# Kernel optimization log

Hardware: AMD Instinct MI355X
Metric: run time of the kernel (lower is better)

## Reference

```python
import jax, jax.numpy as jnp
import numpy as np

B, S, T = 1024, 1024, 32  # batch, seq_len, num_tags


def setup_inputs() -> dict:
    key = jax.random.key(0)
    k1, k2, k3, k4 = jax.random.split(key, 4)
    logits = jax.random.normal(k1, (B, S, T), dtype=jnp.float32)
    transitions = jax.random.normal(k2, (T, T), dtype=jnp.float32)
    tags = jax.random.randint(k3, (B, S), 0, T)
    lengths = jax.random.randint(k4, (B,), 1, S + 1)
    return {"logits": logits, "transitions": transitions, "tags": tags, "lengths": lengths}


def _forward_alg(logits, transitions):
    # viterbi_0 = logits[:, 0, :]; then for t>=1:
    # v_next[b, j] = logsumexp_i(v[b, i] + trans[i, j]) + logits[b, t, j]
    v0 = logits[:, 0, :]  # (B, T)
    emits = jnp.swapaxes(logits[:, 1:, :], 0, 1)  # (S-1, B, T)

    def step(v, emit_t):
        v_next = jax.nn.logsumexp(v[:, :, None] + transitions[None, :, :], axis=1) + emit_t
        return v_next, None

    v_final, _ = jax.lax.scan(step, v0, emits)
    return jax.nn.logsumexp(v_final, axis=1)  # (B,)


def _score_sentence(logits, transitions, tags, lengths):
    # emission scores of gold tags, masked to t < length (note: original ignores
    # lengths in the forward algorithm but uses them here, faithfully reproduced)
    emit = jnp.take_along_axis(logits, tags[:, :, None], axis=2)[..., 0]  # (B, S)
    pos = jnp.arange(S)
    emit_mask = (pos[None, :] < lengths[:, None]).astype(logits.dtype)
    score = jnp.sum(emit * emit_mask, axis=1)
    # transition scores trans[tags[t-1], tags[t]] for 1 <= t < length
    trans_sc = transitions[tags[:, :-1], tags[:, 1:]]  # (B, S-1)
    trans_mask = (pos[None, 1:] < lengths[:, None]).astype(logits.dtype)
    score = score + jnp.sum(trans_sc * trans_mask, axis=1)
    return score  # (B,)


def reference(logits, transitions, tags, lengths):
    log_z = _forward_alg(logits, transitions)
    gold = _score_sentence(logits, transitions, tags, lengths)
    return jnp.mean(log_z - gold)
```

## Files before the change

kernel.cpp:

```cpp
#include <hip/hip_runtime.h>

#define NB 1024
#define NS 1024
#define NT 32
#define L2E 1.44269504088896340736f
#define LN2 0.69314718055994530942f

typedef short        bfrag  __attribute__((ext_vector_type(8)));
typedef float        cfrag  __attribute__((ext_vector_type(16)));
typedef __bf16       bf16x2 __attribute__((ext_vector_type(2)));
typedef float        f32x8  __attribute__((ext_vector_type(8)));
typedef float        f32x4  __attribute__((ext_vector_type(4)));
typedef float        f32x2  __attribute__((ext_vector_type(2)));
typedef unsigned int u32;
typedef unsigned int u32x2v __attribute__((ext_vector_type(2)));
typedef unsigned int u32x4  __attribute__((ext_vector_type(4)));

__device__ __forceinline__ float fexp2(float x){ return __builtin_amdgcn_exp2f(x); }
__device__ __forceinline__ float flog2(float x){ return __builtin_amdgcn_logf(x); }

__device__ __forceinline__ u32 pkbf_rne(float a, float b){
    f32x2 t; t.x = a; t.y = b;
    return __builtin_bit_cast(u32, __builtin_convertvector(t, bf16x2));
}
__device__ __forceinline__ u32 pkbf_t(float a, float b){
    return __builtin_amdgcn_perm(__builtin_bit_cast(u32, b),
                                 __builtin_bit_cast(u32, a), 0x07060302u);
}
__device__ __forceinline__ bfrag mk_afrag(f32x8 v){
    u32x4 r;
    r[0] = pkbf_rne(v[0], v[1]); r[1] = pkbf_rne(v[2], v[3]);
    r[2] = pkbf_rne(v[4], v[5]); r[3] = pkbf_rne(v[6], v[7]);
    return __builtin_bit_cast(bfrag, r);
}

#if __has_builtin(__builtin_amdgcn_permlane32_swap)
#define HAVE_PLSWAP 1
#else
#define HAVE_PLSWAP 0
#endif

__device__ __forceinline__ void half_swap(u32 &x, u32 &y, int h){
#if HAVE_PLSWAP
    u32x2v r = __builtin_amdgcn_permlane32_swap(x, y, false, false);
    x = r[0]; y = r[1];
#else
    u32 X  = __shfl_xor(h ? x : y, 32, 64);
    u32 nx = h ? X : x;
    u32 ny = h ? y : X;
    x = nx; y = ny;
#endif
}

template<int N> struct ic { static constexpr int value = N; };
union accu { cfrag c; f32x2 p[8]; };
union q4u  { f32x4 v; f32x2 p[2]; };

__global__ __launch_bounds__(256, 8) void crf_chunk(
    const float* __restrict__ logits, const float* __restrict__ trans,
    u32* __restrict__ wmat, float* __restrict__ woff)
{
    __shared__ __align__(16) float dscall[4 * 512];

    const int tid = threadIdx.x;
    const int wv  = tid >> 6, lt = tid & 63;
    const int m   = lt & 31,  h  = lt >> 5;
    const int bc  = blockIdx.x * 4 + wv;
    const int b   = bc >> 3,  c  = bc & 7;
    float* dsc = dscall + wv * 512;

    const float* base = logits + (size_t)b * NS * NT;

    f32x8 Et0, Et1;
    #pragma unroll
    for (int j = 0; j < 8; j++){
        Et0[j] = fexp2(L2E * trans[(     8*h + j)*NT + m]);
        Et1[j] = fexp2(L2E * trans[(16 + 8*h + j)*NT + m]);
    }
    const bfrag A0f = mk_afrag(Et0);
    const bfrag A1f = mk_afrag(Et1);

    u32x4 B0v, B1v;
    #pragma unroll
    for (int d = 0; d < 4; d++){
        int k0 = 8*h + 2*d;      u32 v = 0;
        if (k0     == m) v |= 0x3F80u;
        if (k0 + 1 == m) v |= 0x3F800000u;
        B0v[d] = v;
        int k1 = 16 + 8*h + 2*d; v = 0;
        if (k1     == m) v |= 0x3F80u;
        if (k1 + 1 == m) v |= 0x3F800000u;
        B1v[d] = v;
    }

    cfrag zacc;
    #pragma unroll
    for (int q = 0; q < 16; q++) zacc[q] = 0.0f;

    int   offi = 0;
    float exf  = 0.0f;
    const int tbeg = c*128 + 1;

    float eA[4], eB[4];

    auto issue = [&](float (&e)[4], int k){
        const int t0 = tbeg + k*8 + 4*h;
        #pragma unroll
        for (int i = 0; i < 4; i++){
            int t = t0 + i; t = t > (NS-1) ? (NS-1) : t;
            e[i] = base[t*NT + m];
        }
    };
    auto commit = [&](float (&e)[4], int k){
        float* sp = dsc + (k & 1)*256 + (4*h)*32 + m;
        float a0 = (h == 0) ? -exf : 0.0f;
        sp[0]    = fexp2(fmaf(L2E, e[0], a0));
        sp[32]   = fexp2(L2E * e[1]);
        sp[64]   = fexp2(L2E * e[2]);
        sp[96]   = fexp2(L2E * e[3]);
    };

    auto exref = [&](float ref)->int{
        u32 xb = __builtin_bit_cast(u32, ref);
        u32 xf = __builtin_amdgcn_readfirstlane(xb);
        int ex = (int)((xf >> 23) & 0xFFu) - 127;
        return ex < -120 ? -120 : (ex > 120 ? 120 : ex);
    };

    auto procN = [&](int k, bool defer, auto nstc){
        constexpr int NST = decltype(nstc)::value;
        const float* db = dsc + (k & 1)*256 + 4*h;
        #pragma unroll
        for (int i = 0; i < NST; i++){
            accu acc;
            acc.c = __builtin_amdgcn_mfma_f32_32x32x16_bf16(
                        A0f, __builtin_bit_cast(bfrag, B0v), zacc, 0, 0, 0);
            acc.c = __builtin_amdgcn_mfma_f32_32x32x16_bf16(
                        A1f, __builtin_bit_cast(bfrag, B1v), acc.c, 0, 0, 0);

            q4u d0, d1, d2, d3;
            d0.v = *(const f32x4*)(db + i*32 +  0);
            d1.v = *(const f32x4*)(db + i*32 +  8);
            d2.v = *(const f32x4*)(db + i*32 + 16);
            d3.v = *(const f32x4*)(db + i*32 + 24);
            acc.p[0] *= d0.p[0]; acc.p[1] *= d0.p[1];
            acc.p[2] *= d1.p[0]; acc.p[3] *= d1.p[1];
            acc.p[4] *= d2.p[0]; acc.p[5] *= d2.p[1];
            acc.p[6] *= d3.p[0]; acc.p[7] *= d3.p[1];

            if (i == 3){
                int ex = exref(fmaxf(acc.c[0], acc.c[8]));
                offi += ex;
                f32x2 s2;
                s2.x = s2.y = __builtin_bit_cast(float, (u32)(127 - ex) << 23);
                #pragma unroll
                for (int q = 0; q < 8; q++) acc.p[q] *= s2;
            }
            if (i == 7 && defer){
                int ex = exref(fmaxf(acc.c[0], acc.c[8]));
                offi += ex;
                exf = (float)ex;
            }

            u32 P0 = pkbf_t(acc.c[0],  acc.c[1]),  P1 = pkbf_t(acc.c[2],  acc.c[3]);
            u32 P2 = pkbf_t(acc.c[4],  acc.c[5]),  P3 = pkbf_t(acc.c[6],  acc.c[7]);
            u32 P4 = pkbf_t(acc.c[8],  acc.c[9]),  P5 = pkbf_t(acc.c[10], acc.c[11]);
            u32 P6 = pkbf_t(acc.c[12], acc.c[13]), P7 = pkbf_t(acc.c[14], acc.c[15]);
            half_swap(P0, P2, h); half_swap(P1, P3, h);
            half_swap(P4, P6, h); half_swap(P5, P7, h);
            B0v[0]=P0; B0v[1]=P1; B0v[2]=P2; B0v[3]=P3;
            B1v[0]=P4; B1v[1]=P5; B1v[2]=P6; B1v[3]=P7;
        }
    };

    issue(eA, 0); commit(eA, 0);
    #pragma unroll 1
    for (int k = 0; k < 14; k += 2){
        issue(eB, k + 1);
        procN(k, true, ic<8>{});
        commit(eB, k + 1);
        issue(eA, k + 2);
        procN(k + 1, true, ic<8>{});
        commit(eA, k + 2);
    }
    issue(eB, 15);
    procN(14, true, ic<8>{});
    commit(eB, 15);
    if (c != 7) procN(15, false, ic<8>{});
    else        procN(15, false, ic<7>{});

    const size_t mb = (size_t)bc * 512;
    #pragma unroll
    for (int d = 0; d < 4; d++){
        wmat[mb + d*64 + lt]     = B0v[d];
        wmat[mb + (4+d)*64 + lt] = B1v[d];
    }
    if (lt == 0) woff[bc] = (float)offi;
}

__global__ __launch_bounds__(256) void crf_gold(
    const float* __restrict__ logits, const float* __restrict__ trans,
    const int* __restrict__ tags, const int* __restrict__ lens,
    float* __restrict__ out)
{
    __shared__ __align__(16) float ldsT[NT*NT];
    __shared__ __align__(16) int   ldsTag[NS];
    __shared__ float red[4];

    const int tid = threadIdx.x;
    const int b   = blockIdx.x;
    const int len = lens[b];
    const float* lgb = logits + (size_t)b * NS * NT;

    ((float4*)ldsT)[tid]  = ((const float4*)trans)[tid];
    ((int4*)ldsTag)[tid]  = ((const int4*)(tags + (size_t)b * NS))[tid];
    __syncthreads();

    const int t0 = tid * 4;
    int4 tgv = ((const int4*)ldsTag)[tid];
    int  prv = ldsTag[tid == 0 ? 0 : t0 - 1];
    int tgs[5] = {prv, tgv.x, tgv.y, tgv.z, tgv.w};

    float g = 0.0f;
    #pragma unroll
    for (int i = 0; i < 4; i++){
        int t = t0 + i;
        if (t < len){
            float e  = lgb[t*NT + tgs[i+1]];
            float tr = (t >= 1) ? ldsT[tgs[i]*NT + tgs[i+1]] : 0.0f;
            g += e + tr;
        }
    }

    #pragma unroll
    for (int d = 1; d < 64; d <<= 1) g += __shfl_xor(g, d, 64);
    if ((tid & 63) == 0) red[tid >> 6] = g;
    __syncthreads();
    if (tid == 0){
        float gs = red[0] + red[1] + red[2] + red[3];
        atomicAdd(out, -gs * (1.0f / (float)NB));
    }
}

__global__ __launch_bounds__(64) void crf_combine(
    const float* __restrict__ logits,
    const u32* __restrict__ wmat, const float* __restrict__ woff,
    float* __restrict__ out)
{
    __shared__ __align__(16) float ldsU[NT];

    const int tid = threadIdx.x;
    const int m   = tid & 31;
    const int b   = blockIdx.x;
    const float* lgb = logits + (size_t)b * NS * NT;

    float offs[8];
    #pragma unroll
    for (int cc = 0; cc < 8; cc++) offs[cc] = woff[b*8 + cc];

    float v    = fexp2(L2E * lgb[m]);
    float voff = 0.0f;

    const int n  = m;
    const int f  = n >> 4;
    const int hh = (n >> 3) & 1;
    const int di = f*4 + ((n >> 1) & 3);

    auto ldrow = [&](int cc, uint4 (&md)[8]){
        const uint4* mp = (const uint4*)(wmat + (size_t)(b*8 + cc)*512 + di*64 + hh*32);
        #pragma unroll
        for (int qq = 0; qq < 8; qq++) md[qq] = mp[qq];
    };

    uint4 mdA[8], mdB[8];
    ldrow(0, mdA);

    #pragma unroll
    for (int cc = 0; cc < 8; cc++){
        uint4 (&cur)[8] = (cc & 1) ? mdB : mdA;
        uint4 (&nxt)[8] = (cc & 1) ? mdA : mdB;
        if (cc < 7) ldrow(cc + 1, nxt);

        float w  = flog2(v) + offs[cc];
        float mw = w;
        #pragma unroll
        for (int d = 1; d <= 16; d <<= 1) mw = fmaxf(mw, __shfl_xor(mw, d, 64));
        float u = fexp2(w - mw);
        if (tid < 32) ldsU[m] = u;
        __syncthreads();

        float acc = 0.0f;
        #pragma unroll
        for (int qq = 0; qq < 8; qq++){
            uint4  md = cur[qq];
            float4 uu = ((const float4*)ldsU)[qq];
            float e0 = __builtin_bit_cast(float, (n&1) ? (md.x & 0xFFFF0000u) : (md.x << 16));
            float e1 = __builtin_bit_cast(float, (n&1) ? (md.y & 0xFFFF0000u) : (md.y << 16));
            float e2 = __builtin_bit_cast(float, (n&1) ? (md.z & 0xFFFF0000u) : (md.z << 16));
            float e3 = __builtin_bit_cast(float, (n&1) ? (md.w & 0xFFFF0000u) : (md.w << 16));
            acc = fmaf(e0, uu.x, acc);
            acc = fmaf(e1, uu.y, acc);
            acc = fmaf(e2, uu.z, acc);
            acc = fmaf(e3, uu.w, acc);
        }
        v = acc;
        voff += mw;
        __syncthreads();
    }

    float s = v;
    #pragma unroll
    for (int d = 1; d <= 16; d <<= 1) s += __shfl_xor(s, d, 64);
    if (tid == 0){
        float logz = LN2 * (voff + flog2(s));
        atomicAdd(out, logz * (1.0f / (float)NB));
    }
}

extern "C" void kernel_launch(void* const* d_in, const int* in_sizes, int n_in,
                              void* d_out, int out_size, void* d_ws, size_t ws_size,
                              hipStream_t stream) {
    const float* logits = (const float*)d_in[0];
    const float* trans  = (const float*)d_in[1];
    const int*   tags   = (const int*)d_in[2];
    const int*   lens   = (const int*)d_in[3];

    u32*   wmat = (u32*)d_ws;
    float* woff = (float*)(wmat + 8192*512);

    hipMemsetAsync(d_out, 0, sizeof(float), stream);
    crf_chunk  <<<2048, 256, 0, stream>>>(logits, trans, wmat, woff);
    crf_gold   <<<1024, 256, 0, stream>>>(logits, trans, tags, lens, (float*)d_out);
    crf_combine<<<1024,  64, 0, stream>>>(logits, wmat, woff, (float*)d_out);
}
```

Measured before the change: 278.6 us.

## Fuse gold-score into chunk kernel and drop half-swap via permuted tag order

Removes the separate gold-score kernel. Its emission and transition sums are now accumulated inside the chunk kernel from the logits already loaded there, and the per-chunk partials go to a workspace buffer that the combine kernel reads. The tag index is also permuted (rho) in the transition A-fragment, the identity B init and the combine readout. This lets the MFMA output be packed straight back into B operands, dropping the cross-half permlane swaps on the serial recurrence path. The cost is extra scattered tag and transition loads inside the latency-critical chunk loop, plus a reliance on the permutation being exactly right.

Result: slower. 309.0 us (+10.9%).

```diff
diff --git a/kernel.cpp b/kernel.cpp
--- a/kernel.cpp
+++ b/kernel.cpp
@@ -13,7 +13,6 @@
 typedef float        f32x4  __attribute__((ext_vector_type(4)));
 typedef float        f32x2  __attribute__((ext_vector_type(2)));
 typedef unsigned int u32;
-typedef unsigned int u32x2v __attribute__((ext_vector_type(2)));
 typedef unsigned int u32x4  __attribute__((ext_vector_type(4)));
 
 __device__ __forceinline__ float fexp2(float x){ return __builtin_amdgcn_exp2f(x); }
@@ -34,22 +33,9 @@
     return __builtin_bit_cast(bfrag, r);
 }
 
-#if __has_builtin(__builtin_amdgcn_permlane32_swap)
-#define HAVE_PLSWAP 1
-#else
-#define HAVE_PLSWAP 0
-#endif
-
-__device__ __forceinline__ void half_swap(u32 &x, u32 &y, int h){
-#if HAVE_PLSWAP
-    u32x2v r = __builtin_amdgcn_permlane32_swap(x, y, false, false);
-    x = r[0]; y = r[1];
-#else
-    u32 X  = __shfl_xor(h ? x : y, 32, 64);
-    u32 nx = h ? X : x;
-    u32 ny = h ? y : X;
-    x = nx; y = ny;
-#endif
+__device__ __forceinline__ int rho(int k){
+    int bb = (k >> 2) & 3;
+    return (bb == 1 || bb == 2) ? (k ^ 12) : k;
 }
 
 template<int N> struct ic { static constexpr int value = N; };
@@ -58,7 +44,8 @@
 
 __global__ __launch_bounds__(256, 8) void crf_chunk(
     const float* __restrict__ logits, const float* __restrict__ trans,
-    u32* __restrict__ wmat, float* __restrict__ woff)
+    const int* __restrict__ tags, const int* __restrict__ lens,
+    u32* __restrict__ wmat, float* __restrict__ woff, float* __restrict__ gpart)
 {
     __shared__ __align__(16) float dscall[4 * 512];
 
@@ -70,12 +57,14 @@
     float* dsc = dscall + wv * 512;
 
     const float* base = logits + (size_t)b * NS * NT;
+    const int    len  = lens[b];
+    const int    tb   = b * NS;
 
     f32x8 Et0, Et1;
     #pragma unroll
     for (int j = 0; j < 8; j++){
-        Et0[j] = fexp2(L2E * trans[(     8*h + j)*NT + m]);
-        Et1[j] = fexp2(L2E * trans[(16 + 8*h + j)*NT + m]);
+        Et0[j] = fexp2(L2E * trans[rho(     8*h + j)*NT + m]);
+        Et1[j] = fexp2(L2E * trans[rho(16 + 8*h + j)*NT + m]);
     }
     const bfrag A0f = mk_afrag(Et0);
     const bfrag A1f = mk_afrag(Et1);
@@ -84,12 +73,12 @@
     #pragma unroll
     for (int d = 0; d < 4; d++){
         int k0 = 8*h + 2*d;      u32 v = 0;
-        if (k0     == m) v |= 0x3F80u;
-        if (k0 + 1 == m) v |= 0x3F800000u;
+        if (rho(k0)     == m) v |= 0x3F80u;
+        if (rho(k0 + 1) == m) v |= 0x3F800000u;
         B0v[d] = v;
         int k1 = 16 + 8*h + 2*d; v = 0;
-        if (k1     == m) v |= 0x3F80u;
-        if (k1 + 1 == m) v |= 0x3F800000u;
+        if (rho(k1)     == m) v |= 0x3F80u;
+        if (rho(k1 + 1) == m) v |= 0x3F800000u;
         B1v[d] = v;
     }
 
@@ -99,6 +88,7 @@
 
     int   offi = 0;
     float exf  = 0.0f;
+    float g    = 0.0f;
     const int tbeg = c*128 + 1;
 
     float eA[4], eB[4];
@@ -118,6 +108,16 @@
         sp[32]   = fexp2(L2E * e[1]);
         sp[64]   = fexp2(L2E * e[2]);
         sp[96]   = fexp2(L2E * e[3]);
+        const int t0 = tbeg + k*8 + 4*h;
+        int tp = tags[tb + t0 - 1];
+        #pragma unroll
+        for (int i = 0; i < 4; i++){
+            int t  = t0 + i;
+            int tc = tags[tb + (t > (NS-1) ? (NS-1) : t)];
+            float contrib = e[i] + trans[tp*NT + tc];
+            if (t < len && m == tc) g += contrib;
+            tp = tc;
+        }
     };
 
     auto exref = [&](float ref)->int{
@@ -162,14 +162,10 @@
                 exf = (float)ex;
             }
 
-            u32 P0 = pkbf_t(acc.c[0],  acc.c[1]),  P1 = pkbf_t(acc.c[2],  acc.c[3]);
-            u32 P2 = pkbf_t(acc.c[4],  acc.c[5]),  P3 = pkbf_t(acc.c[6],  acc.c[7]);
-            u32 P4 = pkbf_t(acc.c[8],  acc.c[9]),  P5 = pkbf_t(acc.c[10], acc.c[11]);
-            u32 P6 = pkbf_t(acc.c[12], acc.c[13]), P7 = pkbf_t(acc.c[14], acc.c[15]);
-            half_swap(P0, P2, h); half_swap(P1, P3, h);
-            half_swap(P4, P6, h); half_swap(P5, P7, h);
-            B0v[0]=P0; B0v[1]=P1; B0v[2]=P2; B0v[3]=P3;
-            B1v[0]=P4; B1v[1]=P5; B1v[2]=P6; B1v[3]=P7;
+            B0v[0] = pkbf_t(acc.c[0],  acc.c[1]);  B0v[1] = pkbf_t(acc.c[2],  acc.c[3]);
+            B0v[2] = pkbf_t(acc.c[4],  acc.c[5]);  B0v[3] = pkbf_t(acc.c[6],  acc.c[7]);
+            B1v[0] = pkbf_t(acc.c[8],  acc.c[9]);  B1v[1] = pkbf_t(acc.c[10], acc.c[11]);
+            B1v[2] = pkbf_t(acc.c[12], acc.c[13]); B1v[3] = pkbf_t(acc.c[14], acc.c[15]);
         }
     };
 
@@ -196,56 +192,16 @@
         wmat[mb + (4+d)*64 + lt] = B1v[d];
     }
     if (lt == 0) woff[bc] = (float)offi;
-}
-
-__global__ __launch_bounds__(256) void crf_gold(
-    const float* __restrict__ logits, const float* __restrict__ trans,
-    const int* __restrict__ tags, const int* __restrict__ lens,
-    float* __restrict__ out)
-{
-    __shared__ __align__(16) float ldsT[NT*NT];
-    __shared__ __align__(16) int   ldsTag[NS];
-    __shared__ float red[4];
-
-    const int tid = threadIdx.x;
-    const int b   = blockIdx.x;
-    const int len = lens[b];
-    const float* lgb = logits + (size_t)b * NS * NT;
-
-    ((float4*)ldsT)[tid]  = ((const float4*)trans)[tid];
-    ((int4*)ldsTag)[tid]  = ((const int4*)(tags + (size_t)b * NS))[tid];
-    __syncthreads();
-
-    const int t0 = tid * 4;
-    int4 tgv = ((const int4*)ldsTag)[tid];
-    int  prv = ldsTag[tid == 0 ? 0 : t0 - 1];
-    int tgs[5] = {prv, tgv.x, tgv.y, tgv.z, tgv.w};
-
-    float g = 0.0f;
-    #pragma unroll
-    for (int i = 0; i < 4; i++){
-        int t = t0 + i;
-        if (t < len){
-            float e  = lgb[t*NT + tgs[i+1]];
-            float tr = (t >= 1) ? ldsT[tgs[i]*NT + tgs[i+1]] : 0.0f;
-            g += e + tr;
-        }
-    }
 
     #pragma unroll
     for (int d = 1; d < 64; d <<= 1) g += __shfl_xor(g, d, 64);
-    if ((tid & 63) == 0) red[tid >> 6] = g;
-    __syncthreads();
-    if (tid == 0){
-        float gs = red[0] + red[1] + red[2] + red[3];
-        atomicAdd(out, -gs * (1.0f / (float)NB));
-    }
+    if (lt == 0) gpart[bc] = g;
 }
 
 __global__ __launch_bounds__(64) void crf_combine(
-    const float* __restrict__ logits,
+    const float* __restrict__ logits, const int* __restrict__ tags,
     const u32* __restrict__ wmat, const float* __restrict__ woff,
-    float* __restrict__ out)
+    const float* __restrict__ gpart, float* __restrict__ out)
 {
     __shared__ __align__(16) float ldsU[NT];
 
@@ -254,6 +210,14 @@
     const int b   = blockIdx.x;
     const float* lgb = logits + (size_t)b * NS * NT;
 
+    const int   tg0 = tags[(size_t)b * NS];
+    const float e0  = lgb[tg0];
+
+    float4 gp0 = ((const float4*)(gpart + b*8))[0];
+    float4 gp1 = ((const float4*)(gpart + b*8))[1];
+    const float gsum = (gp0.x + gp0.y) + (gp0.z + gp0.w)
+                     + (gp1.x + gp1.y) + (gp1.z + gp1.w);
+
     float offs[8];
     #pragma unroll
     for (int cc = 0; cc < 8; cc++) offs[cc] = woff[b*8 + cc];
@@ -262,9 +226,12 @@
     float voff = 0.0f;
 
     const int n  = m;
-    const int f  = n >> 4;
-    const int hh = (n >> 3) & 1;
-    const int di = f*4 + ((n >> 1) & 3);
+    const int bb = (n >> 2) & 3;
+    const int nn = (bb == 1 || bb == 2) ? (n ^ 12) : n;
+    const int f  = nn >> 4;
+    const int hh = (nn >> 3) & 1;
+    const int di = f*4 + ((nn >> 1) & 3);
+    const int lo = nn & 1;
 
     auto ldrow = [&](int cc, uint4 (&md)[8]){
         const uint4* mp = (const uint4*)(wmat + (size_t)(b*8 + cc)*512 + di*64 + hh*32);
@@ -294,14 +261,14 @@
         for (int qq = 0; qq < 8; qq++){
             uint4  md = cur[qq];
             float4 uu = ((const float4*)ldsU)[qq];
-            float e0 = __builtin_bit_cast(float, (n&1) ? (md.x & 0xFFFF0000u) : (md.x << 16));
-            float e1 = __builtin_bit_cast(float, (n&1) ? (md.y & 0xFFFF0000u) : (md.y << 16));
-            float e2 = __builtin_bit_cast(float, (n&1) ? (md.z & 0xFFFF0000u) : (md.z << 16));
-            float e3 = __builtin_bit_cast(float, (n&1) ? (md.w & 0xFFFF0000u) : (md.w << 16));
-            acc = fmaf(e0, uu.x, acc);
-            acc = fmaf(e1, uu.y, acc);
-            acc = fmaf(e2, uu.z, acc);
-            acc = fmaf(e3, uu.w, acc);
+            float v0 = __builtin_bit_cast(float, lo ? (md.x & 0xFFFF0000u) : (md.x << 16));
+            float v1 = __builtin_bit_cast(float, lo ? (md.y & 0xFFFF0000u) : (md.y << 16));
+            float v2 = __builtin_bit_cast(float, lo ? (md.z & 0xFFFF0000u) : (md.z << 16));
+            float v3 = __builtin_bit_cast(float, lo ? (md.w & 0xFFFF0000u) : (md.w << 16));
+            acc = fmaf(v0, uu.x, acc);
+            acc = fmaf(v1, uu.y, acc);
+            acc = fmaf(v2, uu.z, acc);
+            acc = fmaf(v3, uu.w, acc);
         }
         v = acc;
         voff += mw;
@@ -313,7 +280,7 @@
     for (int d = 1; d <= 16; d <<= 1) s += __shfl_xor(s, d, 64);
     if (tid == 0){
         float logz = LN2 * (voff + flog2(s));
-        atomicAdd(out, logz * (1.0f / (float)NB));
+        atomicAdd(out, (logz - gsum - e0) * (1.0f / (float)NB));
     }
 }
 
@@ -325,11 +292,11 @@
     const int*   tags   = (const int*)d_in[2];
     const int*   lens   = (const int*)d_in[3];
 
-    u32*   wmat = (u32*)d_ws;
-    float* woff = (float*)(wmat + 8192*512);
+    u32*   wmat  = (u32*)d_ws;
+    float* woff  = (float*)(wmat + 8192*512);
+    float* gpart = woff + 8192;
 
     hipMemsetAsync(d_out, 0, sizeof(float), stream);
-    crf_chunk  <<<2048, 256, 0, stream>>>(logits, trans, wmat, woff);
-    crf_gold   <<<1024, 256, 0, stream>>>(logits, trans, tags, lens, (float*)d_out);
-    crf_combine<<<1024,  64, 0, stream>>>(logits, wmat, woff, (float*)d_out);
-}
+    crf_chunk  <<<2048, 256, 0, stream>>>(logits, trans, tags, lens, wmat, woff, gpart);
+    crf_combine<<<1024,  64, 0, stream>>>(logits, tags, wmat, woff, gpart, (float*)d_out);
+}
```
